# Kernel optimization log

Measured on AMD Instinct MI355X. Metric: run time of the kernel, lower is better.

The kernel has to match this reference:

```python
import jax, jax.numpy as jnp
import numpy as np

DIM = 1024
HEADS = 16
HEAD_DIM = DIM // HEADS
HIDDEN = 4 * DIM
EPS = 1e-5


def layer_norm(x, g, b):
    mu = jnp.mean(x, axis=-1, keepdims=True)
    var = jnp.mean(jnp.square(x - mu), axis=-1, keepdims=True)
    return (x - mu) * jax.lax.rsqrt(var + EPS) * g + b


def fast_gelu(x):
    # Ascend fast_gelu == x * sigmoid(1.702 * x)
    return x * jax.nn.sigmoid(1.702 * x)


def setup_inputs() -> dict:
    key = jax.random.key(0)
    ks = jax.random.split(key, 12)
    B, N, C = 16, 577, DIM
    s_in = 1.0 / np.sqrt(DIM)
    s_hid = 1.0 / np.sqrt(HIDDEN)
    return {
        "x": jax.random.normal(ks[0], (B * N, C), jnp.float32),
        "norm1_g": jnp.ones((C,), jnp.float32),
        "norm1_b": jnp.zeros((C,), jnp.float32),
        "Wq": jax.random.normal(ks[1], (C, C), jnp.float32) * s_in,
        "Wk": jax.random.normal(ks[2], (C, C), jnp.float32) * s_in,
        "Wv": jax.random.normal(ks[3], (C, C), jnp.float32) * s_in,
        "Wp": jax.random.normal(ks[4], (C, C), jnp.float32) * s_in,
        "bp": jnp.zeros((C,), jnp.float32),
        "norm2_g": jnp.ones((C,), jnp.float32),
        "norm2_b": jnp.zeros((C,), jnp.float32),
        "W1": jax.random.normal(ks[5], (HIDDEN, C), jnp.float32) * s_in,
        "b1": jnp.zeros((HIDDEN,), jnp.float32),
        "W2": jax.random.normal(ks[6], (C, HIDDEN), jnp.float32) * s_hid,
        "b2": jnp.zeros((C,), jnp.float32),
        "B": B,
        "N": N,
        "C": C,
    }


def reference(x, norm1_g, norm1_b, Wq, Wk, Wv, Wp, bp, norm2_g, norm2_b, W1, b1, W2, b2, B, N, C):
    scale = HEAD_DIM ** -0.5

    h = layer_norm(x, norm1_g, norm1_b)          # [B*N, C]
    # qkv projections (qkv_bias=False), reshape to [B, H, N, D]
    def split_heads(y):
        return y.reshape(B, N, HEADS, HEAD_DIM).transpose(0, 2, 1, 3)

    q = split_heads(h @ Wq.T)
    k = split_heads(h @ Wk.T)
    v = split_heads(h @ Wv.T)

    attn = jnp.einsum('bhqd,bhkd->bhqk', q, k) * scale
    attn = jax.nn.softmax(attn, axis=-1)
    o = jnp.einsum('bhqk,bhkd->bhqd', attn, v)   # [B, H, N, D]
    o = o.transpose(0, 2, 1, 3).reshape(B * N, C)
    y = o @ Wp.T + bp                            # attention output proj

    x = x + y                                    # residual 1 (drop_path=0)
    h2 = layer_norm(x, norm2_g, norm2_b)
    m = fast_gelu(h2 @ W1.T + b1) @ W2.T + b2    # MLP (drop=0)
    return x + m                                 # residual 2
```

## Files before the change

kernel.cpp:

```cpp
#include <hip/hip_runtime.h>

typedef short  short8  __attribute__((ext_vector_type(8)));
typedef float  float4v __attribute__((ext_vector_type(4)));

#define DIM      1024
#define HEADS    16
#define HEAD_DIM 64
#define HIDDEN   4096
#define BATCH    16
#define SEQ      577
#define M_ROWS   (BATCH*SEQ)
#define NPAD2    640
#define QKVLD    3072
#define LOG2E    1.4426950408889634f

static __device__ __forceinline__ unsigned short f2bf(float f) {
  unsigned int u = __float_as_uint(f);
  u += 0x7FFFu + ((u >> 16) & 1u);
  return (unsigned short)(u >> 16);
}
static __device__ __forceinline__ void gload_lds16(const void* g, void* l) {
  __builtin_amdgcn_global_load_lds(
      (const __attribute__((address_space(1))) void*)g,
      (__attribute__((address_space(3))) void*)l, 16, 0, 0);
}
static __device__ __forceinline__ int xcd_chunk(int w, int nwg) {
  int xcd = w & 7, rest = w >> 3;
  int q = nwg >> 3, r = nwg & 7;
  int base = xcd < r ? xcd * (q + 1) : r * (q + 1) + (xcd - r) * q;
  return base + rest;
}

__global__ __launch_bounds__(256) void convert_all_kernel(
    const float* __restrict__ Wq, const float* __restrict__ Wk,
    const float* __restrict__ Wv, const float* __restrict__ Wp,
    const float* __restrict__ W1, const float* __restrict__ W2,
    unsigned short* __restrict__ wqkv, unsigned short* __restrict__ wp,
    unsigned short* __restrict__ w1, unsigned short* __restrict__ w2) {
  const int S = DIM * DIM / 4;
  int i = blockIdx.x * 256 + threadIdx.x;
  const float* src; unsigned short* dst; int rel;
  if (i < 4 * S) {
    if (i < S)        { src = Wq; dst = wqkv;               rel = i; }
    else if (i < 2*S) { src = Wk; dst = wqkv + DIM * DIM;   rel = i - S; }
    else if (i < 3*S) { src = Wv; dst = wqkv + 2*DIM*DIM;   rel = i - 2*S; }
    else              { src = Wp; dst = wp;                 rel = i - 3*S; }
  } else if (i < 8*S) { src = W1; dst = w1;                 rel = i - 4*S; }
  else                { src = W2; dst = w2;                 rel = i - 8*S; }
  float4 v = ((const float4*)src)[rel];
  union { unsigned short s[4]; uint2 u; } p;
  p.s[0] = f2bf(v.x); p.s[1] = f2bf(v.y); p.s[2] = f2bf(v.z); p.s[3] = f2bf(v.w);
  ((uint2*)dst)[rel] = p.u;
}

__global__ __launch_bounds__(256) void ln_kernel(
    const float* __restrict__ x, const float* __restrict__ g,
    const float* __restrict__ b, unsigned short* __restrict__ out) {
  int row = blockIdx.x, tid = threadIdx.x;
  const float* xr = x + (long long)row * DIM;
  float4 v = *(const float4*)(xr + tid * 4);
  float s1 = v.x + v.y + v.z + v.w;
  float s2 = v.x*v.x + v.y*v.y + v.z*v.z + v.w*v.w;
  #pragma unroll
  for (int o = 32; o; o >>= 1) { s1 += __shfl_xor(s1, o); s2 += __shfl_xor(s2, o); }
  __shared__ float a1[4], a2[4];
  int wid = tid >> 6, lane = tid & 63;
  if (lane == 0) { a1[wid] = s1; a2[wid] = s2; }
  __syncthreads();
  s1 = a1[0] + a1[1] + a1[2] + a1[3];
  s2 = a2[0] + a2[1] + a2[2] + a2[3];
  float mean = s1 * (1.f / DIM);
  float var  = s2 * (1.f / DIM) - mean * mean;
  float rstd = rsqrtf(var + 1e-5f);
  float4 gv = *(const float4*)(g + tid * 4);
  float4 bv = *(const float4*)(b + tid * 4);
  union { unsigned short s[4]; uint2 u; } p;
  p.s[0] = f2bf((v.x - mean) * rstd * gv.x + bv.x);
  p.s[1] = f2bf((v.y - mean) * rstd * gv.y + bv.y);
  p.s[2] = f2bf((v.z - mean) * rstd * gv.z + bv.z);
  p.s[3] = f2bf((v.w - mean) * rstd * gv.w + bv.w);
  *(uint2*)(out + (long long)row * DIM + tid * 4) = p.u;
}

__global__ __launch_bounds__(256) void transpose_v_kernel(
    const unsigned short* __restrict__ v, unsigned short* __restrict__ vt) {
  int nt0 = blockIdx.x * 64;
  int bh = blockIdx.y;
  int b = bh >> 4, h = bh & 15;
  __shared__ unsigned short T[64][72];
  int tid = threadIdx.x;
  int r = tid >> 3;
  int c = tid & 7;
  #pragma unroll
  for (int p = 0; p < 2; p++) {
    int row = p * 32 + r;
    int n = nt0 + row;
    uint4 val = (uint4){0u, 0u, 0u, 0u};
    if (n < SEQ)
      val = *(const uint4*)(v + ((long long)(b * SEQ + n)) * QKVLD + h * HEAD_DIM + c * 8);
    *(uint4*)&T[row][c * 8] = val;
  }
  __syncthreads();
  #pragma unroll
  for (int p = 0; p < 2; p++) {
    int d = p * 32 + (tid >> 3);
    union { unsigned short s[8]; uint4 u; } o;
    #pragma unroll
    for (int i = 0; i < 8; i++) o.s[i] = T[c * 8 + i][d];
    *(uint4*)(vt + ((long long)bh * HEAD_DIM + d) * NPAD2 + nt0 + c * 8) = o.u;
  }
}

template <bool MASK>
static __device__ __forceinline__ void attn_tile(
    const unsigned short* Ks, const unsigned short* Vs, unsigned short* Ps,
    const short8 (&af)[2][2], float4v (&oacc)[2][4], float4v (&sumacc)[2],
    int quad, int l16, int wid) {
  const float CE = 0.125f * LOG2E;

  short8 bfr[4][2];
  #pragma unroll
  for (int j = 0; j < 4; j++) {
    int r = j * 16 + l16;
    #pragma unroll
    for (int ks = 0; ks < 2; ks++)
      bfr[j][ks] = *(const short8*)(Ks + r * 64 + ((ks * 4 + quad) ^ (l16 & 7)) * 8);
  }

  float4v sacc[2][4];
  #pragma unroll
  for (int i = 0; i < 2; i++)
    #pragma unroll
    for (int j = 0; j < 4; j++) sacc[i][j] = (float4v){0.f, 0.f, 0.f, 0.f};
  #pragma unroll
  for (int i = 0; i < 2; i++)
    #pragma unroll
    for (int j = 0; j < 4; j++)
      #pragma unroll
      for (int ks = 0; ks < 2; ks++)
        sacc[i][j] = __builtin_amdgcn_mfma_f32_16x16x32_bf16(af[i][ks], bfr[j][ks], sacc[i][j], 0, 0, 0);

  #pragma unroll
  for (int i = 0; i < 2; i++) {
    #pragma unroll
    for (int reg = 0; reg < 4; reg++) {
      int prow = wid * 32 + i * 16 + quad * 4 + reg;
      #pragma unroll
      for (int j = 0; j < 4; j++) {
        float pv;
        if constexpr (MASK) {
          pv = (j == 0 && l16 == 0) ? __builtin_amdgcn_exp2f(sacc[i][j][reg] * CE) : 0.f;
        } else {
          pv = __builtin_amdgcn_exp2f(sacc[i][j][reg] * CE);
        }
        int pcol = j * 16 + l16;
        Ps[prow * 64 + (((pcol >> 3) ^ (prow & 7)) * 8) + (pcol & 7)] = f2bf(pv);
      }
    }
  }

  short8 paf[2][2], vbf[4][2];
  #pragma unroll
  for (int i = 0; i < 2; i++) {
    int r = wid * 32 + i * 16 + l16;
    #pragma unroll
    for (int kk = 0; kk < 2; kk++)
      paf[i][kk] = *(const short8*)(Ps + r * 64 + ((kk * 4 + quad) ^ (l16 & 7)) * 8);
  }
  #pragma unroll
  for (int j = 0; j < 4; j++) {
    int r = j * 16 + l16;
    #pragma unroll
    for (int kk = 0; kk < 2; kk++)
      vbf[j][kk] = *(const short8*)(Vs + r * 64 + ((kk * 4 + quad) ^ (l16 & 7)) * 8);
  }
  const short ov = (short)0x3F80;
  const short8 ones = (short8){ov, ov, ov, ov, ov, ov, ov, ov};
  #pragma unroll
  for (int i = 0; i < 2; i++) {
    #pragma unroll
    for (int kk = 0; kk < 2; kk++) {
      #pragma unroll
      for (int j = 0; j < 4; j++)
        oacc[i][j] = __builtin_amdgcn_mfma_f32_16x16x32_bf16(paf[i][kk], vbf[j][kk], oacc[i][j], 0, 0, 0);
      sumacc[i] = __builtin_amdgcn_mfma_f32_16x16x32_bf16(paf[i][kk], ones, sumacc[i], 0, 0, 0);
    }
  }
}

__global__ __launch_bounds__(256, 3) void flash_attn_kernel(
    const unsigned short* __restrict__ q,
    const unsigned short* __restrict__ k,
    const unsigned short* __restrict__ vt,
    unsigned short* __restrict__ o) {
  int w = blockIdx.y * 5 + blockIdx.x;
  int id = xcd_chunk(w, 5 * 256);
  int qt = id % 5;
  int bh = id / 5;
  int b = bh >> 4, h = bh & 15;
  int q0 = qt * 128;
  int tid = threadIdx.x, lane = tid & 63, wid = tid >> 6;
  int quad = lane >> 4, l16 = lane & 15;
  long long rowbase = (long long)b * SEQ;

  __shared__ __align__(16) unsigned short SM[24576];
  unsigned short* Ps = SM + 16384;

  int sr = wid * 16 + (lane >> 3);
  int scc = (lane & 7) ^ (sr & 7);
  const unsigned short* kbase = k + (rowbase + sr) * QKVLD + h * HEAD_DIM + scc * 8;
  const unsigned short* kbase2 = k + (rowbase + sr + 8) * QKVLD + h * HEAD_DIM + (((lane & 7) ^ ((sr + 8) & 7)) * 8);
  const unsigned short* vbase = vt + ((long long)bh * HEAD_DIM + sr) * NPAD2 + scc * 8;
  const unsigned short* vbase2 = vt + ((long long)bh * HEAD_DIM + sr + 8) * NPAD2 + (((lane & 7) ^ ((sr + 8) & 7)) * 8);

  auto stageKV = [&](int sel, int kt) {
    unsigned short* Ks_ = SM + sel * 8192;
    unsigned short* Vs_ = Ks_ + 4096;
    long long koff = (long long)kt * 64 * QKVLD;
    long long koff2 = koff;
    if (kt == 9) {
      koff  -= (long long)((kt * 64 + sr)     - (SEQ - 1) > 0 ? (kt * 64 + sr)     - (SEQ - 1) : 0) * QKVLD;
      koff2 -= (long long)((kt * 64 + sr + 8) - (SEQ - 1) > 0 ? (kt * 64 + sr + 8) - (SEQ - 1) : 0) * QKVLD;
    }
    gload_lds16(kbase  + koff,  Ks_ + sr * 64 - (lane >> 3) * 64);
    gload_lds16(kbase2 + koff2, Ks_ + (sr + 8) * 64 - (lane >> 3) * 64);
    gload_lds16(vbase  + kt * 64, Vs_ + sr * 64 - (lane >> 3) * 64);
    gload_lds16(vbase2 + kt * 64, Vs_ + (sr + 8) * 64 - (lane >> 3) * 64);
  };

  short8 af[2][2];
  #pragma unroll
  for (int i = 0; i < 2; i++) {
    int gr = q0 + wid * 32 + i * 16 + l16;
    if (gr > SEQ - 1) gr = SEQ - 1;
    const unsigned short* qr = q + (rowbase + gr) * QKVLD + h * HEAD_DIM;
    #pragma unroll
    for (int ks = 0; ks < 2; ks++)
      af[i][ks] = *(const short8*)(qr + (ks * 4 + quad) * 8);
  }

  float4v oacc[2][4];
  float4v sumacc[2];
  #pragma unroll
  for (int i = 0; i < 2; i++) {
    sumacc[i] = (float4v){0.f, 0.f, 0.f, 0.f};
    #pragma unroll
    for (int j = 0; j < 4; j++) oacc[i][j] = (float4v){0.f, 0.f, 0.f, 0.f};
  }

  stageKV(0, 0);

  for (int kt = 0; kt < 10; kt++) {
    int cur = kt & 1;
    if (kt < 9) {
      stageKV(cur ^ 1, kt + 1);
      asm volatile("s_waitcnt vmcnt(4)" ::: "memory");
    } else {
      asm volatile("s_waitcnt vmcnt(0)" ::: "memory");
    }
    __builtin_amdgcn_s_barrier();
    const unsigned short* Ks_ = SM + cur * 8192;
    const unsigned short* Vs_ = Ks_ + 4096;
    if (kt < 9) attn_tile<false>(Ks_, Vs_, Ps, af, oacc, sumacc, quad, l16, wid);
    else        attn_tile<true >(Ks_, Vs_, Ps, af, oacc, sumacc, quad, l16, wid);
    asm volatile("" ::: "memory");
    __builtin_amdgcn_s_barrier();
  }

  #pragma unroll
  for (int i = 0; i < 2; i++) {
    #pragma unroll
    for (int reg = 0; reg < 4; reg++) {
      int grow = q0 + wid * 32 + i * 16 + quad * 4 + reg;
      if (grow >= SEQ) continue;
      float inv = 1.f / sumacc[i][reg];
      #pragma unroll
      for (int j = 0; j < 4; j++) {
        int d = j * 16 + l16;
        o[(rowbase + grow) * DIM + h * HEAD_DIM + d] = f2bf(oacc[i][j][reg] * inv);
      }
    }
  }
}

enum { EPI_BF16 = 0, EPI_BIAS_RES_F32 = 2, EPI_BIAS_GELU_BF16 = 3 };

template <int EPI>
__global__ __launch_bounds__(256, 4) void gemm_nt(
    const unsigned short* __restrict__ A, int lda,
    const unsigned short* __restrict__ B, int ldb,
    void* __restrict__ Cout, int ldc,
    const float* __restrict__ bias, const float* __restrict__ res,
    int M, int N, int K) {
  int mt = gridDim.x, nt = gridDim.y;
  int nwg = mt * nt;
  int id = xcd_chunk(blockIdx.y * mt + blockIdx.x, nwg);
  int band  = id / (8 * nt);
  int rem   = id - band * 8 * nt;
  int mrem  = mt - band * 8;
  int bandh = mrem < 8 ? mrem : 8;
  int lm = rem % bandh;
  int nb = rem / bandh;
  int m0 = (band * 8 + lm) * 128, n0 = nb * 128;

  int tid = threadIdx.x;
  int lane = tid & 63, wid = tid >> 6;
  int wm = wid >> 1, wn = wid & 1;
  int quad = lane >> 4, l16 = lane & 15;

  __shared__ __align__(16) char SMEM[32768];
  unsigned short* As = (unsigned short*)SMEM;
  unsigned short* Bs = As + 128 * 64;

  float4v acc[4][4];
  #pragma unroll
  for (int i = 0; i < 4; i++)
    #pragma unroll
    for (int j = 0; j < 4; j++) acc[i][j] = (float4v){0.f, 0.f, 0.f, 0.f};

  int lr8 = lane >> 3;
  int sc  = ((lane & 7) ^ lr8) * 8;

  const unsigned short* pA[4];
  const unsigned short* pB[4];
  #pragma unroll
  for (int p = 0; p < 4; p++) {
    int ra = wid * 32 + p * 8;
    int gr = m0 + ra + lr8; if (gr > M - 1) gr = M - 1;
    pA[p] = A + (long long)gr * lda + sc;
    int gn = n0 + ra + lr8; if (gn > N - 1) gn = N - 1;
    pB[p] = B + (long long)gn * ldb + sc;
  }

  for (int k0 = 0; k0 < K; k0 += 64) {
    #pragma unroll
    for (int p = 0; p < 4; p++) {
      int ra = wid * 32 + p * 8;
      gload_lds16(pA[p] + k0, As + ra * 64);
      gload_lds16(pB[p] + k0, Bs + ra * 64);
    }
    __syncthreads();
    #pragma unroll
    for (int ks = 0; ks < 2; ks++) {
      short8 af[4], bfr[4];
      #pragma unroll
      for (int i = 0; i < 4; i++)
        af[i]  = *(const short8*)(As + (wm * 64 + i * 16 + l16) * 64 + (((ks * 4 + quad) ^ (l16 & 7)) * 8));
      #pragma unroll
      for (int j = 0; j < 4; j++)
        bfr[j] = *(const short8*)(Bs + (wn * 64 + j * 16 + l16) * 64 + (((ks * 4 + quad) ^ (l16 & 7)) * 8));
      #pragma unroll
      for (int i = 0; i < 4; i++)
        #pragma unroll
        for (int j = 0; j < 4; j++)
          acc[i][j] = __builtin_amdgcn_mfma_f32_16x16x32_bf16(af[i], bfr[j], acc[i][j], 0, 0, 0);
    }
    __syncthreads();
  }

  float* cs = (float*)SMEM + wid * (16 * 68);
  int erow = lane >> 2;
  int eq   = lane & 3;

  #pragma unroll
  for (int i = 0; i < 4; i++) {
    #pragma unroll
    for (int j = 0; j < 4; j++)
      #pragma unroll
      for (int r = 0; r < 4; r++)
        cs[(quad * 4 + r) * 68 + j * 16 + l16] = acc[i][j][r];
    int grow = m0 + wm * 64 + i * 16 + erow;
    bool rowok = grow < M;

    if constexpr (EPI == EPI_BIAS_RES_F32) {
      #pragma unroll
      for (int t = 0; t < 4; t++) {
        int colb = t * 16 + eq * 4;
        int gcol = n0 + wn * 64 + colb;
        if (!rowok || gcol >= N) continue;
        float4 vv = *(const float4*)&cs[erow * 68 + colb];
        float4 bb = *(const float4*)&bias[gcol];
        const float4 rr = *(const float4*)&res[(long long)grow * ldc + gcol];
        vv.x += bb.x + rr.x; vv.y += bb.y + rr.y;
        vv.z += bb.z + rr.z; vv.w += bb.w + rr.w;
        *(float4*)((float*)Cout + (long long)grow * ldc + gcol) = vv;
      }
    } else {
      #pragma unroll
      for (int h = 0; h < 2; h++) {
        int colb = h * 32 + eq * 8;
        int gcol = n0 + wn * 64 + colb;
        if (!rowok || gcol >= N) continue;
        float4 a0 = *(const float4*)&cs[erow * 68 + colb];
        float4 a1 = *(const float4*)&cs[erow * 68 + colb + 4];
        float vs[8] = {a0.x, a0.y, a0.z, a0.w, a1.x, a1.y, a1.z, a1.w};
        if constexpr (EPI == EPI_BIAS_GELU_BF16) {
          float4 b0 = *(const float4*)&bias[gcol];
          float4 b1 = *(const float4*)&bias[gcol + 4];
          float bs[8] = {b0.x, b0.y, b0.z, b0.w, b1.x, b1.y, b1.z, b1.w};
          #pragma unroll
          for (int e = 0; e < 8; e++) {
            float tt = vs[e] + bs[e];
            float ex = __builtin_amdgcn_exp2f(tt * -2.4554669595930156f);
            vs[e] = tt / (1.f + ex);
          }
        }
        union { unsigned short s[8]; uint4 u; } p;
        #pragma unroll
        for (int e = 0; e < 8; e++) p.s[e] = f2bf(vs[e]);
        *(uint4*)((unsigned short*)Cout + (long long)grow * ldc + gcol) = p.u;
      }
    }
  }
}

extern "C" void kernel_launch(void* const* d_in, const int* in_sizes, int n_in,
                              void* d_out, int out_size, void* d_ws, size_t ws_size,
                              hipStream_t stream) {
  const float* x   = (const float*)d_in[0];
  const float* g1  = (const float*)d_in[1];
  const float* be1 = (const float*)d_in[2];
  const float* Wq  = (const float*)d_in[3];
  const float* Wk  = (const float*)d_in[4];
  const float* Wv  = (const float*)d_in[5];
  const float* Wp  = (const float*)d_in[6];
  const float* bp  = (const float*)d_in[7];
  const float* g2  = (const float*)d_in[8];
  const float* be2 = (const float*)d_in[9];
  const float* W1  = (const float*)d_in[10];
  const float* b1  = (const float*)d_in[11];
  const float* W2  = (const float*)d_in[12];
  const float* b2  = (const float*)d_in[13];
  float* out = (float*)d_out;

  char* ws = (char*)d_ws;
  size_t off = 0;
  auto alloc = [&](size_t bytes) {
    size_t r = off; off += (bytes + 255) & ~(size_t)255; return r;
  };
  unsigned short* wqkv_bf = (unsigned short*)(ws + alloc((size_t)3 * DIM * DIM * 2));
  unsigned short* wp_bf   = (unsigned short*)(ws + alloc((size_t)DIM * DIM * 2));
  unsigned short* w1_bf   = (unsigned short*)(ws + alloc((size_t)HIDDEN * DIM * 2));
  unsigned short* w2_bf   = (unsigned short*)(ws + alloc((size_t)HIDDEN * DIM * 2));
  unsigned short* h_bf    = (unsigned short*)(ws + alloc((size_t)M_ROWS * DIM * 2));
  unsigned short* qkv_bf  = (unsigned short*)(ws + alloc((size_t)M_ROWS * QKVLD * 2));
  unsigned short* vt_bf   = (unsigned short*)(ws + alloc((size_t)256 * HEAD_DIM * NPAD2 * 2));

  unsigned short* o_bf  = h_bf;
  unsigned short* h2_bf = h_bf;
  unsigned short* u_bf  = qkv_bf;
  float*          x1    = out;

  convert_all_kernel<<<12 * (DIM * DIM / 4) / 256, 256, 0, stream>>>(
      Wq, Wk, Wv, Wp, W1, W2, wqkv_bf, wp_bf, w1_bf, w2_bf);

  ln_kernel<<<M_ROWS, 256, 0, stream>>>(x, g1, be1, h_bf);

  gemm_nt<EPI_BF16><<<dim3(73, 24), 256, 0, stream>>>(h_bf, DIM, wqkv_bf, DIM,
      qkv_bf, QKVLD, nullptr, nullptr, M_ROWS, 3 * DIM, DIM);

  transpose_v_kernel<<<dim3(10, 256), 256, 0, stream>>>(qkv_bf + 2 * DIM, vt_bf);

  flash_attn_kernel<<<dim3(5, 256), 256, 0, stream>>>(
      qkv_bf, qkv_bf + DIM, vt_bf, o_bf);

  gemm_nt<EPI_BIAS_RES_F32><<<dim3(73, 8), 256, 0, stream>>>(o_bf, DIM, wp_bf, DIM,
      x1, DIM, bp, x, M_ROWS, DIM, DIM);

  ln_kernel<<<M_ROWS, 256, 0, stream>>>(x1, g2, be2, h2_bf);

  gemm_nt<EPI_BIAS_GELU_BF16><<<dim3(73, 32), 256, 0, stream>>>(h2_bf, DIM, w1_bf, DIM,
      u_bf, HIDDEN, b1, nullptr, M_ROWS, HIDDEN, DIM);

  gemm_nt<EPI_BIAS_RES_F32><<<dim3(73, 8), 256, 0, stream>>>(u_bf, HIDDEN, w2_bf, HIDDEN,
      out, DIM, b2, x1, M_ROWS, DIM, HIDDEN);
}
```

Measured before the change: 502.7 us.

## Enlarge GEMM tiles to 256x256 with a 4-stage async LDS pipeline

The bf16 GEMM now uses 512-thread blocks computing 256x256 tiles with K-steps of 32, instead of 256 threads on 128x128 tiles. Global-to-LDS loads run through a four-buffer ring with explicit vmcnt waits, so loads for later steps overlap MFMA work on the current one, and s_setprio raises priority around the MFMA blocks. The intent is more data reuse per tile and hidden load latency. The cost is 128 KB of LDS and 8x4 accumulators per wave, which cuts occupancy, and larger tiles mean coarser wave quantization on the 9232-row M dimension. The N bounds check in the epilogue was dropped, which relies on N being a multiple of 256.

```diff
diff --git a/kernel.cpp b/kernel.cpp
--- a/kernel.cpp
+++ b/kernel.cpp
@@ -286,7 +286,7 @@
 enum { EPI_BF16 = 0, EPI_BIAS_RES_F32 = 2, EPI_BIAS_GELU_BF16 = 3 };
 
 template <int EPI>
-__global__ __launch_bounds__(256, 4) void gemm_nt(
+__global__ __launch_bounds__(512, 2) void gemm_nt(
     const unsigned short* __restrict__ A, int lda,
     const unsigned short* __restrict__ B, int ldb,
     void* __restrict__ Cout, int ldc,
@@ -301,75 +301,108 @@
   int bandh = mrem < 8 ? mrem : 8;
   int lm = rem % bandh;
   int nb = rem / bandh;
-  int m0 = (band * 8 + lm) * 128, n0 = nb * 128;
+  int m0 = (band * 8 + lm) * 256, n0 = nb * 256;
 
   int tid = threadIdx.x;
   int lane = tid & 63, wid = tid >> 6;
-  int wm = wid >> 1, wn = wid & 1;
+  int wm = wid >> 2, wn = wid & 3;
   int quad = lane >> 4, l16 = lane & 15;
 
-  __shared__ __align__(16) char SMEM[32768];
-  unsigned short* As = (unsigned short*)SMEM;
-  unsigned short* Bs = As + 128 * 64;
-
-  float4v acc[4][4];
-  #pragma unroll
-  for (int i = 0; i < 4; i++)
+  __shared__ __align__(16) unsigned short SMB[65536];
+
+  float4v acc[8][4];
+  #pragma unroll
+  for (int i = 0; i < 8; i++)
     #pragma unroll
     for (int j = 0; j < 4; j++) acc[i][j] = (float4v){0.f, 0.f, 0.f, 0.f};
 
-  int lr8 = lane >> 3;
-  int sc  = ((lane & 7) ^ lr8) * 8;
-
-  const unsigned short* pA[4];
-  const unsigned short* pB[4];
-  #pragma unroll
-  for (int p = 0; p < 4; p++) {
-    int ra = wid * 32 + p * 8;
-    int gr = m0 + ra + lr8; if (gr > M - 1) gr = M - 1;
-    pA[p] = A + (long long)gr * lda + sc;
-    int gn = n0 + ra + lr8; if (gn > N - 1) gn = N - 1;
-    pB[p] = B + (long long)gn * ldb + sc;
-  }
-
-  for (int k0 = 0; k0 < K; k0 += 64) {
-    #pragma unroll
-    for (int p = 0; p < 4; p++) {
-      int ra = wid * 32 + p * 8;
-      gload_lds16(pA[p] + k0, As + ra * 64);
-      gload_lds16(pB[p] + k0, Bs + ra * 64);
-    }
-    __syncthreads();
-    #pragma unroll
-    for (int ks = 0; ks < 2; ks++) {
-      short8 af[4], bfr[4];
-      #pragma unroll
-      for (int i = 0; i < 4; i++)
-        af[i]  = *(const short8*)(As + (wm * 64 + i * 16 + l16) * 64 + (((ks * 4 + quad) ^ (l16 & 7)) * 8));
-      #pragma unroll
-      for (int j = 0; j < 4; j++)
-        bfr[j] = *(const short8*)(Bs + (wn * 64 + j * 16 + l16) * 64 + (((ks * 4 + quad) ^ (l16 & 7)) * 8));
-      #pragma unroll
-      for (int i = 0; i < 4; i++)
-        #pragma unroll
-        for (int j = 0; j < 4; j++)
-          acc[i][j] = __builtin_amdgcn_mfma_f32_16x16x32_bf16(af[i], bfr[j], acc[i][j], 0, 0, 0);
-    }
-    __syncthreads();
-  }
-
-  float* cs = (float*)SMEM + wid * (16 * 68);
+  int srow = wid * 32 + (lane >> 2);
+  int sc   = (((lane & 3) ^ ((lane >> 2) & 3))) * 8;
+  const unsigned short* pA[2];
+  const unsigned short* pB[2];
+  #pragma unroll
+  for (int ii = 0; ii < 2; ii++) {
+    int gr = m0 + srow + ii * 16; if (gr > M - 1) gr = M - 1;
+    pA[ii] = A + (long long)gr * lda + sc;
+    int gn = n0 + srow + ii * 16; if (gn > N - 1) gn = N - 1;
+    pB[ii] = B + (long long)gn * ldb + sc;
+  }
+
+  auto stage = [&](int u) {
+    unsigned short* As_ = SMB + (u & 3) * 16384;
+    unsigned short* Bs_ = As_ + 8192;
+    int k0 = u << 5;
+    #pragma unroll
+    for (int ii = 0; ii < 2; ii++) {
+      int rbase = (wid * 32 + ii * 16) * 32;
+      gload_lds16(pA[ii] + k0, As_ + rbase);
+      gload_lds16(pB[ii] + k0, Bs_ + rbase);
+    }
+  };
+
+  int rsw = (quad ^ (l16 & 3)) << 3;
+  auto compute = [&](int u) {
+    const unsigned short* As_ = SMB + (u & 3) * 16384;
+    const unsigned short* Bs_ = As_ + 8192;
+    short8 a[8], b[4];
+    #pragma unroll
+    for (int mi = 0; mi < 8; mi++)
+      a[mi] = *(const short8*)(As_ + (wm * 128 + mi * 16 + l16) * 32 + rsw);
+    #pragma unroll
+    for (int ni = 0; ni < 4; ni++)
+      b[ni] = *(const short8*)(Bs_ + (wn * 64 + ni * 16 + l16) * 32 + rsw);
+    __builtin_amdgcn_s_setprio(1);
+    #pragma unroll
+    for (int mi = 0; mi < 8; mi++)
+      #pragma unroll
+      for (int ni = 0; ni < 4; ni++)
+        acc[mi][ni] = __builtin_amdgcn_mfma_f32_16x16x32_bf16(a[mi], b[ni], acc[mi][ni], 0, 0, 0);
+    __builtin_amdgcn_s_setprio(0);
+  };
+
+  int U = K >> 5;
+  stage(0); stage(1); stage(2);
+
+  for (int p = 0; p < U - 3; p++) {
+    stage(p + 3);
+    asm volatile("s_waitcnt vmcnt(12)" ::: "memory");
+    __builtin_amdgcn_s_barrier();
+    __builtin_amdgcn_sched_barrier(0);
+    compute(p);
+    __builtin_amdgcn_sched_barrier(0);
+    __builtin_amdgcn_s_barrier();
+  }
+  asm volatile("s_waitcnt vmcnt(8)" ::: "memory");
+  __builtin_amdgcn_s_barrier();
+  __builtin_amdgcn_sched_barrier(0);
+  compute(U - 3);
+  __builtin_amdgcn_sched_barrier(0);
+  __builtin_amdgcn_s_barrier();
+  asm volatile("s_waitcnt vmcnt(4)" ::: "memory");
+  __builtin_amdgcn_s_barrier();
+  __builtin_amdgcn_sched_barrier(0);
+  compute(U - 2);
+  __builtin_amdgcn_sched_barrier(0);
+  __builtin_amdgcn_s_barrier();
+  asm volatile("s_waitcnt vmcnt(0)" ::: "memory");
+  __builtin_amdgcn_s_barrier();
+  __builtin_amdgcn_sched_barrier(0);
+  compute(U - 1);
+  __builtin_amdgcn_sched_barrier(0);
+  __builtin_amdgcn_s_barrier();
+
+  float* cs = (float*)SMB + wid * (16 * 68);
   int erow = lane >> 2;
   int eq   = lane & 3;
 
   #pragma unroll
-  for (int i = 0; i < 4; i++) {
-    #pragma unroll
-    for (int j = 0; j < 4; j++)
+  for (int mi = 0; mi < 8; mi++) {
+    #pragma unroll
+    for (int ni = 0; ni < 4; ni++)
       #pragma unroll
       for (int r = 0; r < 4; r++)
-        cs[(quad * 4 + r) * 68 + j * 16 + l16] = acc[i][j][r];
-    int grow = m0 + wm * 64 + i * 16 + erow;
+        cs[(quad * 4 + r) * 68 + ni * 16 + l16] = acc[mi][ni][r];
+    int grow = m0 + wm * 128 + mi * 16 + erow;
     bool rowok = grow < M;
 
     if constexpr (EPI == EPI_BIAS_RES_F32) {
@@ -377,7 +410,7 @@
       for (int t = 0; t < 4; t++) {
         int colb = t * 16 + eq * 4;
         int gcol = n0 + wn * 64 + colb;
-        if (!rowok || gcol >= N) continue;
+        if (!rowok) continue;
         float4 vv = *(const float4*)&cs[erow * 68 + colb];
         float4 bb = *(const float4*)&bias[gcol];
         const float4 rr = *(const float4*)&res[(long long)grow * ldc + gcol];
@@ -390,7 +423,7 @@
       for (int h = 0; h < 2; h++) {
         int colb = h * 32 + eq * 8;
         int gcol = n0 + wn * 64 + colb;
-        if (!rowok || gcol >= N) continue;
+        if (!rowok) continue;
         float4 a0 = *(const float4*)&cs[erow * 68 + colb];
         float4 a1 = *(const float4*)&cs[erow * 68 + colb + 4];
         float vs[8] = {a0.x, a0.y, a0.z, a0.w, a1.x, a1.y, a1.z, a1.w};
@@ -456,7 +489,7 @@
 
   ln_kernel<<<M_ROWS, 256, 0, stream>>>(x, g1, be1, h_bf);
 
-  gemm_nt<EPI_BF16><<<dim3(73, 24), 256, 0, stream>>>(h_bf, DIM, wqkv_bf, DIM,
+  gemm_nt<EPI_BF16><<<dim3(37, 12), 512, 0, stream>>>(h_bf, DIM, wqkv_bf, DIM,
       qkv_bf, QKVLD, nullptr, nullptr, M_ROWS, 3 * DIM, DIM);
 
   transpose_v_kernel<<<dim3(10, 256), 256, 0, stream>>>(qkv_bf + 2 * DIM, vt_bf);
@@ -464,14 +497,14 @@
   flash_attn_kernel<<<dim3(5, 256), 256, 0, stream>>>(
       qkv_bf, qkv_bf + DIM, vt_bf, o_bf);
 
-  gemm_nt<EPI_BIAS_RES_F32><<<dim3(73, 8), 256, 0, stream>>>(o_bf, DIM, wp_bf, DIM,
+  gemm_nt<EPI_BIAS_RES_F32><<<dim3(37, 4), 512, 0, stream>>>(o_bf, DIM, wp_bf, DIM,
       x1, DIM, bp, x, M_ROWS, DIM, DIM);
 
   ln_kernel<<<M_ROWS, 256, 0, stream>>>(x1, g2, be2, h2_bf);
 
-  gemm_nt<EPI_BIAS_GELU_BF16><<<dim3(73, 32), 256, 0, stream>>>(h2_bf, DIM, w1_bf, DIM,
+  gemm_nt<EPI_BIAS_GELU_BF16><<<dim3(37, 16), 512, 0, stream>>>(h2_bf, DIM, w1_bf, DIM,
       u_bf, HIDDEN, b1, nullptr, M_ROWS, HIDDEN, DIM);
 
-  gemm_nt<EPI_BIAS_RES_F32><<<dim3(73, 8), 256, 0, stream>>>(u_bf, HIDDEN, w2_bf, HIDDEN,
+  gemm_nt<EPI_BIAS_RES_F32><<<dim3(37, 4), 512, 0, stream>>>(u_bf, HIDDEN, w2_bf, HIDDEN,
       out, DIM, b2, x1, M_ROWS, DIM, HIDDEN);
 }
```

Measured after the change: 584.8 us. 16.3% more time.
